# Optimization experiments

Hardware: AMD Instinct MI355X
Metric: run time of the kernel (lower is better)

The kernel has to match this reference:

```python
import jax, jax.numpy as jnp
import numpy as np
import math

H, W = 512, 1024
PS = 2
H_p, W_p = H // PS, W // PS
N = 9
C_IN, C_OUT = 128, 64
GROUPS = 32
B = 2
EPS_GN = 1e-5


def _make_grid():
    # Replicates LatDeform2xDown buffers: centers + sec(lat)-scaled 3x3 offsets.
    pr = np.arange(H_p, dtype=np.float32) * PS + (PS - 1) / 2
    pc = np.arange(W_p, dtype=np.float32) * PS + (PS - 1) / 2
    cy = pr / (H - 1) * 2 - 1
    cx = pc / (W - 1) * 2 - 1
    centers = np.stack([np.broadcast_to(cx[None, :], (H_p, W_p)),
                        np.broadcast_to(cy[:, None], (H_p, W_p))], axis=-1)  # (H_p,W_p,2)
    delta = math.pi / (H - 1)  # drop_south_pole = False
    lat = math.pi / 2 - pr * delta
    sec_max = W / 4.0
    sec = np.clip(1.0 / np.cos(lat), -sec_max, sec_max).astype(np.float32)
    ky, kx = np.meshgrid(np.array([-1.0, 0.0, 1.0], np.float32),
                         np.array([-1.0, 0.0, 1.0], np.float32), indexing='ij')
    kxf, kyf = kx.flatten(), ky.flatten()
    dx = (kxf[None, :] * sec[:, None]) / (W - 1) * 2          # (H_p, 9)
    dy = np.broadcast_to(kyf[None, :], (H_p, N)) / (H - 1) * 2  # (H_p, 9)
    offsets = np.stack([dx, dy], axis=-1)                      # (H_p, 9, 2)
    locs = centers[:, :, None, :] + offsets[:, None, :, :]     # (H_p, W_p, 9, 2)
    return jnp.asarray(locs.reshape(-1, 2).astype(np.float32))


def group_norm(x, gamma, beta, groups, eps=EPS_GN):
    b, c, h, w = x.shape
    xg = x.reshape(b, groups, c // groups, h, w)
    mu = xg.mean(axis=(2, 3, 4), keepdims=True)
    var = ((xg - mu) ** 2).mean(axis=(2, 3, 4), keepdims=True)
    xn = ((xg - mu) * jax.lax.rsqrt(var + eps)).reshape(b, c, h, w)
    return xn * gamma[None, :, None, None] + beta[None, :, None, None]


def setup_inputs() -> dict:
    key = jax.random.key(0)
    ks = jax.random.split(key, 3)
    x = jax.random.normal(ks[0], (B, C_IN, H_p, W_p), dtype=jnp.float32)
    w_conv = jax.random.normal(ks[1], (N * C_OUT, C_IN), dtype=jnp.float32) * 0.02
    w_post = jax.random.normal(ks[2], (C_OUT, C_OUT), dtype=jnp.float32) * 0.05
    return {
        'x': x,
        'grid': _make_grid(),
        'gamma1': jnp.ones((C_IN,), jnp.float32),
        'beta1': jnp.zeros((C_IN,), jnp.float32),
        'w_conv': w_conv,
        'splat_bias': jnp.zeros((C_OUT,), jnp.float32),
        'w_post': w_post,
        'b_post': jnp.zeros((C_OUT,), jnp.float32),
        'gamma2': jnp.ones((C_OUT,), jnp.float32),
        'beta2': jnp.zeros((C_OUT,), jnp.float32),
    }


def reference(x, grid, gamma1, beta1, w_conv, splat_bias, w_post, b_post, gamma2, beta2):
    b = x.shape[0]
    # norm + 1x1 conv (no bias): Wx part of the Wx+b split
    h = group_norm(x, gamma1, beta1, GROUPS)
    vals = jnp.einsum('oc,bchw->bohw', w_conv, h)                 # (B, 9*C, H_p, W_p)
    vals = vals.reshape(b, C_OUT, N, H_p, W_p).transpose(0, 1, 3, 4, 2)
    vals = vals.reshape(b, C_OUT, H_p * W_p * N)                  # (B, C, M)

    # bilinear splat coordinates
    px = (grid[:, 0] + 1.0) * 0.5 * (W - 1)                       # (M,)
    py = (grid[:, 1] + 1.0) * 0.5 * (H - 1)
    x0 = jnp.floor(px).astype(jnp.int32)
    y0 = jnp.floor(py).astype(jnp.int32)
    x1, y1 = x0 + 1, y0 + 1
    fx = px - x0.astype(px.dtype)
    fy = py - y0.astype(py.dtype)
    w00 = (1 - fx) * (1 - fy)
    w01 = (1 - fx) * fy
    w10 = fx * (1 - fy)
    w11 = fx * fy
    x0w = x0 % W
    x1w = x1 % W
    half_W = W // 2

    def polar_wrap(yi, xi):
        past_n = yi < 0
        past_s = yi >= H
        yi = jnp.where(past_n, -yi, yi)
        yi = jnp.where(past_s, 2 * H - yi, yi)
        xi = jnp.where(past_n | past_s, (xi + half_W) % W, xi)
        return jnp.clip(yi, 0, H - 1), xi

    num = jnp.zeros((b, C_OUT, H * W), x.dtype)
    den = jnp.zeros((H * W,), x.dtype)  # identical across batch in the original
    for wt, yi, xi in ((w00, y0, x0w), (w01, y1, x0w), (w10, y0, x1w), (w11, y1, x1w)):
        yi, xi = polar_wrap(yi, xi)
        idx = yi * W + xi                                          # (M,)
        num = num.at[:, :, idx].add(vals * wt[None, None, :])
        den = den.at[idx].add(wt)

    out = num / jnp.clip(den, 1e-8)[None, None, :]
    out = out.reshape(b, C_OUT, H, W) + splat_bias[None, :, None, None]
    # post: 1x1 conv + GroupNorm + exact GELU
    out = jnp.einsum('oc,bchw->bohw', w_post, out) + b_post[None, :, None, None]
    out = group_norm(out, gamma2, beta2, GROUPS)
    return jax.nn.gelu(out, approximate=False)
```

## Files before the change

kernel.cpp:

```cpp
#include <hip/hip_runtime.h>
#include <cstdint>
#include <cstddef>

#define H_   512
#define W_   1024
#define HP_  256
#define WP_  512
#define NTAP 9
#define CIN  128
#define COUT 64
#define HWP  (HP_*WP_)
#define MIDX (HWP*NTAP)
#define HW_  (H_*W_)

typedef __attribute__((ext_vector_type(8))) short bhalf8_t;
typedef __attribute__((ext_vector_type(4))) float floatx4_t;

__device__ __forceinline__ unsigned short f2bf(float f) {
    unsigned u = __float_as_uint(f);
    u += 0x7fffu + ((u >> 16) & 1u);
    return (unsigned short)(u >> 16);
}
__device__ __forceinline__ float bf2f(unsigned short s) {
    return __uint_as_float(((unsigned)s) << 16);
}

__global__ __launch_bounds__(256) void k0_prep(
    const float* __restrict__ w_conv, const float* __restrict__ w_post,
    unsigned short* __restrict__ w2, unsigned short* __restrict__ wpostbf,
    float* __restrict__ gnzero ) {
    int idx = blockIdx.x * 256 + threadIdx.x;
    if (idx < 576*128) {
        int r = idx >> 7, c = idx & 127;
        int o = r / 9, n = r % 9;
        w2[((n*64 + o) << 7) + c] = f2bf(w_conv[idx]);
    } else if (idx < 576*128 + 4096) {
        int i2 = idx - 576*128;
        wpostbf[i2] = f2bf(w_post[i2]);
    } else if (idx < 576*128 + 4096 + 256) {
        gnzero[idx - (576*128 + 4096)] = 0.f;
    }
}

__global__ __launch_bounds__(256) void k1_stats(const float* __restrict__ x,
                                                float* __restrict__ gnsum1) {
    __shared__ float red[512];
    int bid = blockIdx.x;
    int b = bid >> 8, rem = bid & 255;
    int g = rem >> 3, slice = rem & 7;
    const float4* xp = (const float4*)x + (size_t)(b*CIN + g*4) * (HWP/4) + (size_t)slice*16384;
    float s = 0.f, s2 = 0.f;
    for (int i = threadIdx.x; i < 16384; i += 256) {
        float4 v = xp[i];
        s  += v.x + v.y + v.z + v.w;
        s2 += v.x*v.x + v.y*v.y + v.z*v.z + v.w*v.w;
    }
    red[threadIdx.x] = s; red[256 + threadIdx.x] = s2;
    __syncthreads();
    for (int off = 128; off > 0; off >>= 1) {
        if (threadIdx.x < off) {
            red[threadIdx.x] += red[threadIdx.x + off];
            red[256 + threadIdx.x] += red[256 + threadIdx.x + off];
        }
        __syncthreads();
    }
    if (threadIdx.x == 0) {
        atomicAdd(&gnsum1[(b*32 + g)*2],     red[0]);
        atomicAdd(&gnsum1[(b*32 + g)*2 + 1], red[256]);
    }
}

__global__ void k1b_coef(const float* __restrict__ gnsum1,
                         const float* __restrict__ gamma1, const float* __restrict__ beta1,
                         float* __restrict__ acoef, float* __restrict__ bcoef) {
    int t = threadIdx.x;
    int b = t >> 7, c = t & 127, g = c >> 2;
    float s1 = gnsum1[(b*32+g)*2], s2 = gnsum1[(b*32+g)*2+1];
    const float inv = 1.f / 524288.f;
    float mean = s1 * inv;
    float var  = s2 * inv - mean*mean;
    float rstd = rsqrtf(var + 1e-5f);
    float a = gamma1[c] * rstd;
    acoef[t] = a;
    bcoef[t] = beta1[c] - mean * a;
}

__global__ __launch_bounds__(256) void k2_conv(
    const float* __restrict__ x, const unsigned short* __restrict__ w2,
    const float* __restrict__ acoef, const float* __restrict__ bcoef,
    unsigned short* __restrict__ vals) {
    __shared__ unsigned short As[64*136];
    __shared__ unsigned short Bs[128*136];
    __shared__ unsigned short Cs[128*72];
    int b   = blockIdx.y;
    int tile = blockIdx.x;
    int pr  = tile >> 2, pcb = (tile & 3) << 7;
    int tid = threadIdx.x;

    for (int task = tid; task < 2048; task += 256) {
        int p = task & 127, c0 = (task >> 7) << 3;
        bhalf8_t t8;
        #pragma unroll
        for (int j = 0; j < 8; ++j) {
            int c = c0 + j;
            float xv = x[(size_t)(b*CIN + c)*HWP + (size_t)pr*WP_ + pcb + p];
            float v = fmaf(xv, acoef[b*CIN + c], bcoef[b*CIN + c]);
            t8[j] = (short)f2bf(v);
        }
        *(bhalf8_t*)&Bs[p*136 + c0] = t8;
    }
    __syncthreads();

    int wave = tid >> 6, lane = tid & 63;
    int l15 = lane & 15, lq = lane >> 4;

    bhalf8_t bfr[2][4];
    #pragma unroll
    for (int ptl = 0; ptl < 2; ++ptl) {
        int p = (wave*2 + ptl)*16 + l15;
        #pragma unroll
        for (int ks = 0; ks < 4; ++ks)
            bfr[ptl][ks] = *(const bhalf8_t*)&Bs[p*136 + ks*32 + lq*8];
    }

    for (int n = 0; n < 9; ++n) {
        __syncthreads();
        for (int i = tid; i < 4096; i += 256) {
            int r = i >> 6, cp = i & 63;
            ((unsigned*)As)[r*68 + cp] = ((const unsigned*)w2)[(n*64 + r)*64 + cp];
        }
        __syncthreads();
        floatx4_t acc[2][4] = {};
        #pragma unroll
        for (int ks = 0; ks < 4; ++ks) {
            bhalf8_t af[4];
            #pragma unroll
            for (int rt = 0; rt < 4; ++rt)
                af[rt] = *(const bhalf8_t*)&As[(rt*16 + l15)*136 + ks*32 + lq*8];
            #pragma unroll
            for (int ptl = 0; ptl < 2; ++ptl)
                #pragma unroll
                for (int rt = 0; rt < 4; ++rt)
                    acc[ptl][rt] = __builtin_amdgcn_mfma_f32_16x16x32_bf16(
                        af[rt], bfr[ptl][ks], acc[ptl][rt], 0, 0, 0);
        }
        #pragma unroll
        for (int ptl = 0; ptl < 2; ++ptl) {
            int p = (wave*2 + ptl)*16 + l15;
            #pragma unroll
            for (int rt = 0; rt < 4; ++rt)
                #pragma unroll
                for (int reg = 0; reg < 4; ++reg) {
                    int o = rt*16 + lq*4 + reg;
                    Cs[p*72 + o] = f2bf(acc[ptl][rt][reg]);
                }
        }
        __syncthreads();
        size_t outbase = (size_t)b*HWP + (size_t)pr*WP_ + pcb;
        for (int i = tid; i < 4096; i += 256) {
            int p = i >> 5, o2 = i & 31;
            ((unsigned*)vals)[((outbase + p)*576 + n*64)/2 + o2] = ((const unsigned*)Cs)[p*36 + o2];
        }
    }
}

__global__ __launch_bounds__(256) void k3_gather(
    const float* __restrict__ gridp, const unsigned short* __restrict__ vals,
    const unsigned short* __restrict__ wpostbf,
    const float* __restrict__ splat_bias, const float* __restrict__ b_post,
    float* __restrict__ out, float* __restrict__ gnsum2) {

    __shared__ unsigned short SM[256*72];
    __shared__ unsigned short WPs[64*72];
    __shared__ float sb_s[64], bp_s[64], gsum[64];

    int tid = threadIdx.x;
    int bx = blockIdx.x;
    int y  = blockIdx.y;
    int b  = blockIdx.z;
    int x  = (bx << 8) + tid;

    if (tid < 64) { sb_s[tid] = splat_bias[tid]; bp_s[tid] = b_post[tid]; gsum[tid] = 0.f; }
    for (int i = tid; i < 2048; i += 256) {
        int r = i >> 5, cp = i & 31;
        ((unsigned*)WPs)[r*36 + cp] = ((const unsigned*)wpostbf)[(r << 5) + cp];
    }

    float num[64];
    #pragma unroll
    for (int c = 0; c < 64; ++c) num[c] = 0.f;
    float den = 0.f;

    const float2* g2 = (const float2*)gridp;
    int prc = y >> 1;
    for (int dpr = -1; dpr <= 1; ++dpr) {
        int pr = prc + dpr;
        if (pr < 0 || pr > HP_-1) continue;
        for (int kyi = 0; kyi < 3; ++kyi) {
            float gy = g2[pr*WP_*9 + kyi*3 + 1].y;
            float py = ((gy + 1.0f) * 0.5f) * 511.0f;
            float y0f = floorf(py);
            float fy = py - y0f;
            int y0i = (int)y0f;
            #pragma unroll
            for (int side = 0; side < 2; ++side) {
                int yi = y0i + side;
                bool pn = yi < 0, ps = yi >= H_;
                int yy = pn ? -yi : (ps ? (2*H_ - yi) : yi);
                yy = min(max(yy, 0), H_-1);
                if (yy != y) continue;
                int sh = (pn || ps) ? (W_/2) : 0;
                float wy = side ? fy : (1.0f - fy);
                for (int kxi = 0; kxi < 3; ++kxi) {
                    int n = kyi*3 + kxi;
                    float gx0 = g2[pr*WP_*9 + n].x;
                    float px0 = ((gx0 + 1.0f) * 0.5f) * 1023.0f;
                    int Tt = x - sh - 1;
                    #pragma unroll
                    for (int j = -1; j <= 1; ++j) {
                        float A = ((float)(Tt + j*W_) - px0) * 0.5f;
                        int clo = (int)ceilf(A - 1e-3f);
                        int chi = (int)floorf(A + 1.001f);
                        for (int pc = clo; pc <= chi; ++pc) {
                            if (pc < 0 || pc >= WP_) continue;
                            int m = (pr*WP_ + pc)*9 + n;
                            float2 g = g2[m];
                            float px = ((g.x + 1.0f) * 0.5f) * 1023.0f;
                            float x0f = floorf(px);
                            float fx = px - x0f;
                            int x0i = (int)x0f;
                            int xl = (x0i + 2*W_ + sh) & (W_-1);
                            float w;
                            if (xl == x)                      w = (1.0f - fx) * wy;
                            else if (((xl + 1) & (W_-1)) == x) w = fx * wy;
                            else continue;
                            den += w;
                            const uint4* vp = (const uint4*)(vals + (((size_t)b*MIDX + m) << 6));
                            #pragma unroll
                            for (int q = 0; q < 8; ++q) {
                                uint4 u = vp[q];
                                unsigned uu[4] = {u.x, u.y, u.z, u.w};
                                #pragma unroll
                                for (int e = 0; e < 4; ++e) {
                                    float lo = __uint_as_float(uu[e] << 16);
                                    float hi = __uint_as_float(uu[e] & 0xffff0000u);
                                    num[q*8 + e*2]     = fmaf(w, lo, num[q*8 + e*2]);
                                    num[q*8 + e*2 + 1] = fmaf(w, hi, num[q*8 + e*2 + 1]);
                                }
                            }
                        }
                    }
                }
            }
        }
    }

    float invd = 1.0f / fmaxf(den, 1e-8f);
    {
        int base = tid * 72;
        #pragma unroll
        for (int c8 = 0; c8 < 8; ++c8) {
            bhalf8_t t8;
            #pragma unroll
            for (int jj = 0; jj < 8; ++jj) {
                float v = fmaf(num[c8*8 + jj], invd, sb_s[c8*8 + jj]);
                t8[jj] = (short)f2bf(v);
            }
            *(bhalf8_t*)&SM[base + c8*8] = t8;
        }
    }
    __syncthreads();

    int wave = tid >> 6, lane = tid & 63, l15 = lane & 15, lq = lane >> 4;
    floatx4_t acc[4][4] = {};
    #pragma unroll
    for (int ks = 0; ks < 2; ++ks) {
        bhalf8_t af[4], bf[4];
        #pragma unroll
        for (int ot = 0; ot < 4; ++ot)
            af[ot] = *(const bhalf8_t*)&WPs[(ot*16 + l15)*72 + ks*32 + lq*8];
        #pragma unroll
        for (int pt = 0; pt < 4; ++pt)
            bf[pt] = *(const bhalf8_t*)&SM[((wave*4 + pt)*16 + l15)*72 + ks*32 + lq*8];
        #pragma unroll
        for (int pt = 0; pt < 4; ++pt)
            #pragma unroll
            for (int ot = 0; ot < 4; ++ot)
                acc[pt][ot] = __builtin_amdgcn_mfma_f32_16x16x32_bf16(
                    af[ot], bf[pt], acc[pt][ot], 0, 0, 0);
    }

    float s1l[8], s2l[8];
    #pragma unroll
    for (int li = 0; li < 8; ++li) { s1l[li] = 0.f; s2l[li] = 0.f; }
    #pragma unroll
    for (int pt = 0; pt < 4; ++pt) {
        int px = (wave*4 + pt)*16 + l15;
        int xg = (bx << 8) + px;
        #pragma unroll
        for (int ot = 0; ot < 4; ++ot)
            #pragma unroll
            for (int reg = 0; reg < 4; ++reg) {
                int o = ot*16 + lq*4 + reg;
                float v = acc[pt][ot][reg] + bp_s[o];
                out[((size_t)(b*64 + o) << 19) + ((size_t)y << 10) + xg] = v;
                int li = ot*2 + (reg >> 1);
                s1l[li] += v;
                s2l[li] += v*v;
            }
    }
    #pragma unroll
    for (int li = 0; li < 8; ++li) {
        int g = (li >> 1)*8 + lq*2 + (li & 1);
        atomicAdd(&gsum[g*2],     s1l[li]);
        atomicAdd(&gsum[g*2 + 1], s2l[li]);
    }
    __syncthreads();
    if (tid < 64) atomicAdd(&gnsum2[b*64 + tid], gsum[tid]);
}

__global__ __launch_bounds__(256) void k5_final(
    float* __restrict__ out, const float* __restrict__ gnsum2,
    const float* __restrict__ gamma2, const float* __restrict__ beta2) {
    size_t idx = (size_t)blockIdx.x * 256 + threadIdx.x;
    size_t e8 = idx << 3;
    int b = (int)(e8 >> 25);
    int o = (int)((e8 >> 19) & 63);
    int g = o >> 1;
    float s1 = gnsum2[b*64 + g*2], s2 = gnsum2[b*64 + g*2 + 1];
    const float invn = 1.0f / 1048576.0f;
    float mean = s1 * invn;
    float var  = s2 * invn - mean*mean;
    float rstd = rsqrtf(var + 1e-5f);
    float sc = gamma2[o] * rstd;
    float sf = beta2[o] - mean * sc;
    float4* p0 = (float4*)(out + e8);
    float4 v0 = p0[0], v1 = p0[1];
    float r[8] = {v0.x, v0.y, v0.z, v0.w, v1.x, v1.y, v1.z, v1.w};
    #pragma unroll
    for (int j = 0; j < 8; ++j) {
        float t = fmaf(r[j], sc, sf);
        r[j] = 0.5f * t * (1.0f + erff(t * 0.70710678118654752f));
    }
    p0[0] = make_float4(r[0], r[1], r[2], r[3]);
    p0[1] = make_float4(r[4], r[5], r[6], r[7]);
}

extern "C" void kernel_launch(void* const* d_in, const int* in_sizes, int n_in,
                              void* d_out, int out_size, void* d_ws, size_t ws_size,
                              hipStream_t stream) {
    const float* x      = (const float*)d_in[0];
    const float* gridp  = (const float*)d_in[1];
    const float* gamma1 = (const float*)d_in[2];
    const float* beta1  = (const float*)d_in[3];
    const float* w_conv = (const float*)d_in[4];
    const float* sbias  = (const float*)d_in[5];
    const float* w_post = (const float*)d_in[6];
    const float* b_post = (const float*)d_in[7];
    const float* gamma2 = (const float*)d_in[8];
    const float* beta2  = (const float*)d_in[9];
    float* out = (float*)d_out;

    char* ws = (char*)d_ws;
    unsigned short* w2      = (unsigned short*)(ws);
    unsigned short* wpostbf = (unsigned short*)(ws + 147456);
    float* gnsum1 = (float*)(ws + 155648);
    float* gnsum2 = (float*)(ws + 156160);
    float* acoef  = (float*)(ws + 156672);
    float* bcoef  = (float*)(ws + 157696);
    unsigned short* vals = (unsigned short*)(ws + 158720);

    hipLaunchKernelGGL(k0_prep,  dim3(305),          dim3(256), 0, stream,
                       w_conv, w_post, w2, wpostbf, gnsum1);
    hipLaunchKernelGGL(k1_stats, dim3(512),          dim3(256), 0, stream, x, gnsum1);
    hipLaunchKernelGGL(k1b_coef, dim3(1),            dim3(256), 0, stream,
                       gnsum1, gamma1, beta1, acoef, bcoef);
    hipLaunchKernelGGL(k2_conv,  dim3(1024, 2),      dim3(256), 0, stream,
                       x, w2, acoef, bcoef, vals);
    hipLaunchKernelGGL(k3_gather, dim3(4, 512, 2),   dim3(256), 0, stream,
                       gridp, vals, wpostbf, sbias, b_post, out, gnsum2);
    hipLaunchKernelGGL(k5_final, dim3(32768),        dim3(256), 0, stream,
                       out, gnsum2, gamma2, beta2);
}
```

Measured before the change: 993.6 us.

## Split gather channels across waves, read conv weights from global, shard GN atomics

```diff
diff --git a/kernel.cpp b/kernel.cpp
--- a/kernel.cpp
+++ b/kernel.cpp
@@ -20,9 +20,6 @@
     unsigned u = __float_as_uint(f);
     u += 0x7fffu + ((u >> 16) & 1u);
     return (unsigned short)(u >> 16);
-}
-__device__ __forceinline__ float bf2f(unsigned short s) {
-    return __uint_as_float(((unsigned)s) << 16);
 }
 
 __global__ __launch_bounds__(256) void k0_prep(
@@ -37,7 +34,7 @@
     } else if (idx < 576*128 + 4096) {
         int i2 = idx - 576*128;
         wpostbf[i2] = f2bf(w_post[i2]);
-    } else if (idx < 576*128 + 4096 + 256) {
+    } else if (idx < 576*128 + 4096 + 1152) {
         gnzero[idx - (576*128 + 4096)] = 0.f;
     }
 }
@@ -89,7 +86,6 @@
     const float* __restrict__ x, const unsigned short* __restrict__ w2,
     const float* __restrict__ acoef, const float* __restrict__ bcoef,
     unsigned short* __restrict__ vals) {
-    __shared__ unsigned short As[64*136];
     __shared__ unsigned short Bs[128*136];
     __shared__ unsigned short Cs[128*72];
     int b   = blockIdx.y;
@@ -124,19 +120,13 @@
     }
 
     for (int n = 0; n < 9; ++n) {
-        __syncthreads();
-        for (int i = tid; i < 4096; i += 256) {
-            int r = i >> 6, cp = i & 63;
-            ((unsigned*)As)[r*68 + cp] = ((const unsigned*)w2)[(n*64 + r)*64 + cp];
-        }
-        __syncthreads();
         floatx4_t acc[2][4] = {};
         #pragma unroll
         for (int ks = 0; ks < 4; ++ks) {
             bhalf8_t af[4];
             #pragma unroll
             for (int rt = 0; rt < 4; ++rt)
-                af[rt] = *(const bhalf8_t*)&As[(rt*16 + l15)*136 + ks*32 + lq*8];
+                af[rt] = *(const bhalf8_t*)&w2[(size_t)(n*64 + rt*16 + l15)*128 + ks*32 + lq*8];
             #pragma unroll
             for (int ptl = 0; ptl < 2; ++ptl)
                 #pragma unroll
@@ -144,6 +134,7 @@
                     acc[ptl][rt] = __builtin_amdgcn_mfma_f32_16x16x32_bf16(
                         af[rt], bfr[ptl][ks], acc[ptl][rt], 0, 0, 0);
         }
+        __syncthreads();
         #pragma unroll
         for (int ptl = 0; ptl < 2; ++ptl) {
             int p = (wave*2 + ptl)*16 + l15;
@@ -170,7 +161,7 @@
     const float* __restrict__ splat_bias, const float* __restrict__ b_post,
     float* __restrict__ out, float* __restrict__ gnsum2) {
 
-    __shared__ unsigned short SM[256*72];
+    __shared__ unsigned short SM[64*72];
     __shared__ unsigned short WPs[64*72];
     __shared__ float sb_s[64], bp_s[64], gsum[64];
 
@@ -178,7 +169,9 @@
     int bx = blockIdx.x;
     int y  = blockIdx.y;
     int b  = blockIdx.z;
-    int x  = (bx << 8) + tid;
+    int pxl = tid & 63;
+    int cs  = tid >> 6;
+    int x  = (bx << 6) + pxl;
 
     if (tid < 64) { sb_s[tid] = splat_bias[tid]; bp_s[tid] = b_post[tid]; gsum[tid] = 0.f; }
     for (int i = tid; i < 2048; i += 256) {
@@ -186,9 +179,9 @@
         ((unsigned*)WPs)[r*36 + cp] = ((const unsigned*)wpostbf)[(r << 5) + cp];
     }
 
-    float num[64];
-    #pragma unroll
-    for (int c = 0; c < 64; ++c) num[c] = 0.f;
+    float num[16];
+    #pragma unroll
+    for (int c = 0; c < 16; ++c) num[c] = 0.f;
     float den = 0.f;
 
     const float2* g2 = (const float2*)gridp;
@@ -235,18 +228,15 @@
                             else if (((xl + 1) & (W_-1)) == x) w = fx * wy;
                             else continue;
                             den += w;
-                            const uint4* vp = (const uint4*)(vals + (((size_t)b*MIDX + m) << 6));
+                            const uint4* vp = (const uint4*)(vals + (((size_t)b*MIDX + m) << 6) + (cs << 4));
+                            uint4 u0 = vp[0], u1 = vp[1];
+                            unsigned uu[8] = {u0.x, u0.y, u0.z, u0.w, u1.x, u1.y, u1.z, u1.w};
                             #pragma unroll
-                            for (int q = 0; q < 8; ++q) {
-                                uint4 u = vp[q];
-                                unsigned uu[4] = {u.x, u.y, u.z, u.w};
-                                #pragma unroll
-                                for (int e = 0; e < 4; ++e) {
-                                    float lo = __uint_as_float(uu[e] << 16);
-                                    float hi = __uint_as_float(uu[e] & 0xffff0000u);
-                                    num[q*8 + e*2]     = fmaf(w, lo, num[q*8 + e*2]);
-                                    num[q*8 + e*2 + 1] = fmaf(w, hi, num[q*8 + e*2 + 1]);
-                                }
+                            for (int e = 0; e < 8; ++e) {
+                                float lo = __uint_as_float(uu[e] << 16);
+                                float hi = __uint_as_float(uu[e] & 0xffff0000u);
+                                num[e*2]     = fmaf(w, lo, num[e*2]);
+                                num[e*2 + 1] = fmaf(w, hi, num[e*2 + 1]);
                             }
                         }
                     }
@@ -257,13 +247,14 @@
 
     float invd = 1.0f / fmaxf(den, 1e-8f);
     {
-        int base = tid * 72;
-        #pragma unroll
-        for (int c8 = 0; c8 < 8; ++c8) {
+        int base = pxl * 72 + cs * 16;
+        #pragma unroll
+        for (int c8 = 0; c8 < 2; ++c8) {
             bhalf8_t t8;
             #pragma unroll
             for (int jj = 0; jj < 8; ++jj) {
-                float v = fmaf(num[c8*8 + jj], invd, sb_s[c8*8 + jj]);
+                int c = cs*16 + c8*8 + jj;
+                float v = fmaf(num[c8*8 + jj], invd, sb_s[c]);
                 t8[jj] = (short)f2bf(v);
             }
             *(bhalf8_t*)&SM[base + c8*8] = t8;
@@ -271,44 +262,35 @@
     }
     __syncthreads();
 
-    int wave = tid >> 6, lane = tid & 63, l15 = lane & 15, lq = lane >> 4;
-    floatx4_t acc[4][4] = {};
+    int lane = tid & 63, l15 = lane & 15, lq = lane >> 4;
+    int wave = cs;
+    floatx4_t acc[4] = {};
     #pragma unroll
     for (int ks = 0; ks < 2; ++ks) {
-        bhalf8_t af[4], bf[4];
-        #pragma unroll
-        for (int ot = 0; ot < 4; ++ot)
-            af[ot] = *(const bhalf8_t*)&WPs[(ot*16 + l15)*72 + ks*32 + lq*8];
-        #pragma unroll
-        for (int pt = 0; pt < 4; ++pt)
-            bf[pt] = *(const bhalf8_t*)&SM[((wave*4 + pt)*16 + l15)*72 + ks*32 + lq*8];
-        #pragma unroll
-        for (int pt = 0; pt < 4; ++pt)
-            #pragma unroll
-            for (int ot = 0; ot < 4; ++ot)
-                acc[pt][ot] = __builtin_amdgcn_mfma_f32_16x16x32_bf16(
-                    af[ot], bf[pt], acc[pt][ot], 0, 0, 0);
+        bhalf8_t bf = *(const bhalf8_t*)&SM[(wave*16 + l15)*72 + ks*32 + lq*8];
+        #pragma unroll
+        for (int ot = 0; ot < 4; ++ot) {
+            bhalf8_t af = *(const bhalf8_t*)&WPs[(ot*16 + l15)*72 + ks*32 + lq*8];
+            acc[ot] = __builtin_amdgcn_mfma_f32_16x16x32_bf16(af, bf, acc[ot], 0, 0, 0);
+        }
     }
 
     float s1l[8], s2l[8];
     #pragma unroll
     for (int li = 0; li < 8; ++li) { s1l[li] = 0.f; s2l[li] = 0.f; }
-    #pragma unroll
-    for (int pt = 0; pt < 4; ++pt) {
-        int px = (wave*4 + pt)*16 + l15;
-        int xg = (bx << 8) + px;
-        #pragma unroll
-        for (int ot = 0; ot < 4; ++ot)
-            #pragma unroll
-            for (int reg = 0; reg < 4; ++reg) {
-                int o = ot*16 + lq*4 + reg;
-                float v = acc[pt][ot][reg] + bp_s[o];
-                out[((size_t)(b*64 + o) << 19) + ((size_t)y << 10) + xg] = v;
-                int li = ot*2 + (reg >> 1);
-                s1l[li] += v;
-                s2l[li] += v*v;
-            }
-    }
+    int px = wave*16 + l15;
+    int xg = (bx << 6) + px;
+    #pragma unroll
+    for (int ot = 0; ot < 4; ++ot)
+        #pragma unroll
+        for (int reg = 0; reg < 4; ++reg) {
+            int o = ot*16 + lq*4 + reg;
+            float v = acc[ot][reg] + bp_s[o];
+            out[((size_t)(b*64 + o) << 19) + ((size_t)y << 10) + xg] = v;
+            int li = ot*2 + (reg >> 1);
+            s1l[li] += v;
+            s2l[li] += v*v;
+        }
     #pragma unroll
     for (int li = 0; li < 8; ++li) {
         int g = (li >> 1)*8 + lq*2 + (li & 1);
@@ -316,7 +298,7 @@
         atomicAdd(&gsum[g*2 + 1], s2l[li]);
     }
     __syncthreads();
-    if (tid < 64) atomicAdd(&gnsum2[b*64 + tid], gsum[tid]);
+    if (tid < 64) atomicAdd(&gnsum2[(((b << 6) + tid) << 3) + ((bx + y) & 7)], gsum[tid]);
 }
 
 __global__ __launch_bounds__(256) void k5_final(
@@ -327,7 +309,10 @@
     int b = (int)(e8 >> 25);
     int o = (int)((e8 >> 19) & 63);
     int g = o >> 1;
-    float s1 = gnsum2[b*64 + g*2], s2 = gnsum2[b*64 + g*2 + 1];
+    float s1 = 0.f, s2 = 0.f;
+    int base = ((b*64 + g*2) << 3);
+    #pragma unroll
+    for (int s = 0; s < 8; ++s) { s1 += gnsum2[base + s]; s2 += gnsum2[base + 8 + s]; }
     const float invn = 1.0f / 1048576.0f;
     float mean = s1 * invn;
     float var  = s2 * invn - mean*mean;
@@ -366,18 +351,18 @@
     unsigned short* wpostbf = (unsigned short*)(ws + 147456);
     float* gnsum1 = (float*)(ws + 155648);
     float* gnsum2 = (float*)(ws + 156160);
-    float* acoef  = (float*)(ws + 156672);
-    float* bcoef  = (float*)(ws + 157696);
-    unsigned short* vals = (unsigned short*)(ws + 158720);
-
-    hipLaunchKernelGGL(k0_prep,  dim3(305),          dim3(256), 0, stream,
+    float* acoef  = (float*)(ws + 160256);
+    float* bcoef  = (float*)(ws + 161280);
+    unsigned short* vals = (unsigned short*)(ws + 162304);
+
+    hipLaunchKernelGGL(k0_prep,  dim3(309),          dim3(256), 0, stream,
                        w_conv, w_post, w2, wpostbf, gnsum1);
     hipLaunchKernelGGL(k1_stats, dim3(512),          dim3(256), 0, stream, x, gnsum1);
     hipLaunchKernelGGL(k1b_coef, dim3(1),            dim3(256), 0, stream,
                        gnsum1, gamma1, beta1, acoef, bcoef);
     hipLaunchKernelGGL(k2_conv,  dim3(1024, 2),      dim3(256), 0, stream,
                        x, w2, acoef, bcoef, vals);
-    hipLaunchKernelGGL(k3_gather, dim3(4, 512, 2),   dim3(256), 0, stream,
+    hipLaunchKernelGGL(k3_gather, dim3(16, 512, 2),  dim3(256), 0, stream,
                        gridp, vals, wpostbf, sbias, b_post, out, gnsum2);
     hipLaunchKernelGGL(k5_final, dim3(32768),        dim3(256), 0, stream,
                        out, gnsum2, gamma2, beta2);
```

New measurement: 1.188 ms. +19.6%, slower.
